# Performance work log

Hardware: AMD Instinct MI355X
Metric: run time of the kernel (lower is better)

Reference implementation:

```python
import jax, jax.numpy as jnp
import numpy as np

S, D_IN, D_OUT = 4096, 1024, 1024

def setup_inputs() -> dict:
    key = jax.random.key(0)
    kx, kq, kk, kv = jax.random.split(key, 4)
    scale = 0.02
    return {
        "x": jax.random.normal(kx, (S, D_IN), dtype=jnp.float32),
        "W_query": jax.random.normal(kq, (D_IN, D_OUT), dtype=jnp.float32) * scale,
        "W_key": jax.random.normal(kk, (D_IN, D_OUT), dtype=jnp.float32) * scale,
        "W_value": jax.random.normal(kv, (D_IN, D_OUT), dtype=jnp.float32) * scale,
    }

def reference(x, W_query, W_key, W_value):
    # x: [S, d_in]; W_*: [d_in, d_out]
    queries = x @ W_query        # [S, d_out]
    keys = x @ W_key             # [S, d_out]
    values = x @ W_value         # [S, d_out]
    d_k = keys.shape[-1]
    attn_scores = queries @ keys.T            # [S, S]
    attn_weights = jax.nn.softmax(attn_scores / jnp.sqrt(jnp.float32(d_k)), axis=-1)
    context_vec = attn_weights @ values       # [S, d_out]
    return context_vec
```

## Files before the change

kernel.cpp:

```cpp
#include <hip/hip_runtime.h>

typedef _Float16 f16x8 __attribute__((ext_vector_type(8)));
typedef float f32x4 __attribute__((ext_vector_type(4)));
typedef unsigned short u16;
typedef u16 u16x8 __attribute__((ext_vector_type(8)));
typedef u16 u16x4 __attribute__((ext_vector_type(4)));

__device__ __forceinline__ u16 f2h_bits(float f) {
    _Float16 h = (_Float16)f;
    return __builtin_bit_cast(u16, h);
}
__device__ __forceinline__ float h2f(u16 b) {
    return (float)__builtin_bit_cast(_Float16, b);
}

typedef __attribute__((address_space(1))) unsigned int gu32_as1;
typedef __attribute__((address_space(3))) unsigned int lu32_as3;
__device__ __forceinline__ void gload16(const u16* g, u16* l) {
    __builtin_amdgcn_global_load_lds((gu32_as1*)g, (lu32_as3*)l, 16, 0, 0);
}

template <int MODE>
__global__ __launch_bounds__(512, 2) void gemm_bt(
    const u16* __restrict__ A, int lda,
    const u16* __restrict__ B, int ldb,
    u16* __restrict__ C, int ldc,
    int Ksplit, float alpha, size_t c_z_stride,
    int bnW, int bmW, int numPanelX,
    float* __restrict__ rowsum, u16* __restrict__ vt)
{
    __shared__ __attribute__((aligned(16))) u16 As[32768];
    __shared__ __attribute__((aligned(16))) u16 Bs[32768];

    const int t    = threadIdx.x;
    const int lane = t & 63;
    const int wave = t >> 6;
    const int wm   = wave >> 2;
    const int wn   = wave & 3;
    const int l16  = lane & 15;
    const int quad = lane >> 4;

    const int lin = blockIdx.y * gridDim.x + blockIdx.x;
    const int xcd = lin & 7;
    const int idx = lin >> 3;
    const int px  = xcd % numPanelX;
    const int py  = xcd / numPanelX;
    const int bn  = px * bnW + idx % bnW;
    const int bm  = py * bmW + idx / bnW;

    const int kz = blockIdx.z;
    A += (size_t)kz * Ksplit;
    B += (size_t)kz * Ksplit;
    C += (size_t)kz * c_z_stride;

    const int srow = t >> 2;
    const int sseg = ((t & 3) ^ ((t >> 3) & 3)) * 8;

    const u16* Ag = A + (size_t)(bm * 256 + srow) * lda + sseg;
    const u16* Bg = B + (size_t)(bn * 256 + srow) * ldb + sseg;
    const size_t a128 = (size_t)128 * lda;
    const size_t b128 = (size_t)128 * ldb;

    u16* AsD = &As[t * 8];
    u16* BsD = &Bs[t * 8];

#define STAGE(bufv, kt) do {                                       \
        const u16* _ga = Ag + (size_t)(kt) * 32;                   \
        const u16* _gb = Bg + (size_t)(kt) * 32;                   \
        u16* _la = AsD + (bufv) * 8192;                            \
        u16* _lb = BsD + (bufv) * 8192;                            \
        gload16(_ga,        _la);              \
        gload16(_ga + a128, _la + 4096);       \
        gload16(_gb,        _lb);              \
        gload16(_gb + b128, _lb + 4096);       \
    } while (0)

    const int fslot = (quad ^ ((l16 >> 1) & 3)) * 8;
    const u16* Afr = &As[wm * 4096 + l16 * 32 + fslot];
    const u16* Bfr = &Bs[wn * 2048 + l16 * 32 + fslot];

    f32x4 acc[8][4] = {};

    const int NT = Ksplit >> 5;

    STAGE(0, 0);
    STAGE(1, 1);
    STAGE(2, 2);
    asm volatile("s_waitcnt vmcnt(8)" ::: "memory");
    __builtin_amdgcn_s_barrier();
    asm volatile("" ::: "memory");

    for (int k = 0; k < NT; ++k) {
        const int buf = k & 3;

        f16x8 af[8], bf[4];
#pragma unroll
        for (int mi = 0; mi < 8; mi++)
            af[mi] = *(const f16x8*)(Afr + buf * 8192 + mi * 512);
#pragma unroll
        for (int nj = 0; nj < 4; nj++)
            bf[nj] = *(const f16x8*)(Bfr + buf * 8192 + nj * 512);

        if (k + 3 < NT) STAGE((k + 3) & 3, k + 3);

#pragma unroll
        for (int mi = 0; mi < 8; mi++)
#pragma unroll
            for (int nj = 0; nj < 4; nj++)
                acc[mi][nj] = __builtin_amdgcn_mfma_f32_16x16x32_f16(
                    af[mi], bf[nj], acc[mi][nj], 0, 0, 0);

        if (k < NT - 3)       asm volatile("s_waitcnt vmcnt(8)" ::: "memory");
        else if (k == NT - 3) asm volatile("s_waitcnt vmcnt(4)" ::: "memory");
        else if (k == NT - 2) asm volatile("s_waitcnt vmcnt(0)" ::: "memory");
        __builtin_amdgcn_s_barrier();
        asm volatile("" ::: "memory");
    }
#undef STAGE

    const int crow = bm * 256 + wm * 128 + quad * 4;
    const int ccol = bn * 256 + wn * 64 + l16;

    if (MODE == 1) {
        float rs[8][4];
#pragma unroll
        for (int mi = 0; mi < 8; mi++)
#pragma unroll
            for (int r = 0; r < 4; r++) rs[mi][r] = 0.f;
#pragma unroll
        for (int mi = 0; mi < 8; mi++) {
#pragma unroll
            for (int ni = 0; ni < 4; ni++) {
#pragma unroll
                for (int r = 0; r < 4; r++) {
                    float e = __expf(acc[mi][ni][r] * alpha);
                    rs[mi][r] += e;
                    C[(size_t)(crow + mi * 16 + r) * ldc + (ccol + ni * 16)] = f2h_bits(e);
                }
            }
        }
#pragma unroll
        for (int mi = 0; mi < 8; mi++) {
#pragma unroll
            for (int r = 0; r < 4; r++) {
                float s = rs[mi][r];
#pragma unroll
                for (int o = 1; o < 16; o <<= 1) s += __shfl_xor(s, o);
                if (l16 == 0)
                    atomicAdd(&rowsum[crow + mi * 16 + r], s);
            }
        }
    } else if (MODE == 2 && bn >= 8) {
#pragma unroll
        for (int ni = 0; ni < 4; ni++) {
            const int cV = (bn - 8) * 256 + wn * 64 + ni * 16 + l16;
#pragma unroll
            for (int mi = 0; mi < 8; mi++) {
                u16x4 o;
#pragma unroll
                for (int r = 0; r < 4; r++) o[r] = f2h_bits(acc[mi][ni][r]);
                *(u16x4*)(vt + (size_t)cV * 4096 + crow + mi * 16) = o;
            }
        }
    } else {
#pragma unroll
        for (int mi = 0; mi < 8; mi++)
#pragma unroll
            for (int ni = 0; ni < 4; ni++)
#pragma unroll
                for (int r = 0; r < 4; r++)
                    C[(size_t)(crow + mi * 16 + r) * ldc + (ccol + ni * 16)] =
                        f2h_bits(acc[mi][ni][r] * alpha);
    }
}

__global__ __launch_bounds__(256) void cast_to_f16(
    const float* __restrict__ in, u16* __restrict__ out, int n)
{
    int i = (blockIdx.x * 256 + threadIdx.x) * 4;
    if (i + 3 < n) {
        float4 v = *(const float4*)(in + i);
        ushort4 o;
        o.x = f2h_bits(v.x);
        o.y = f2h_bits(v.y);
        o.z = f2h_bits(v.z);
        o.w = f2h_bits(v.w);
        *(ushort4*)(out + i) = o;
    }
}

__global__ __launch_bounds__(256) void transpose_w3(
    const float* __restrict__ W0, const float* __restrict__ W1,
    const float* __restrict__ W2, u16* __restrict__ out)
{
    const float* in = (blockIdx.z == 0) ? W0 : (blockIdx.z == 1) ? W1 : W2;
    u16* o = out + (size_t)blockIdx.z * 1024 * 1024;
    __shared__ float tile[32][33];
    const int bx = blockIdx.x * 32;
    const int by = blockIdx.y * 32;
    const int tx = threadIdx.x, ty = threadIdx.y;
#pragma unroll
    for (int j = 0; j < 4; j++)
        tile[ty + j * 8][tx] = in[(size_t)(by + ty + j * 8) * 1024 + bx + tx];
    __syncthreads();
#pragma unroll
    for (int j = 0; j < 4; j++)
        o[(size_t)(bx + ty + j * 8) * 1024 + by + tx] = f2h_bits(tile[tx][ty + j * 8]);
}

__global__ __launch_bounds__(256) void zero_f32(float* __restrict__ p, int n)
{
    int i = (blockIdx.x * 256 + threadIdx.x) * 4;
    if (i + 3 < n) *(float4*)(p + i) = float4{0.f, 0.f, 0.f, 0.f};
}

__global__ __launch_bounds__(256) void add_div4(
    const u16* __restrict__ P, const float* __restrict__ l,
    float* __restrict__ o)
{
    const size_t zs = (size_t)4096 * 1024;
    int i = (blockIdx.x * 256 + threadIdx.x) * 8;
    float inv = 1.0f / l[i >> 10];
    float s[8] = {};
#pragma unroll
    for (int z = 0; z < 4; z++) {
        u16x8 h = *(const u16x8*)(P + z * zs + i);
#pragma unroll
        for (int j = 0; j < 8; j++) s[j] += h2f(h[j]);
    }
    float4 lo{s[0] * inv, s[1] * inv, s[2] * inv, s[3] * inv};
    float4 hi{s[4] * inv, s[5] * inv, s[6] * inv, s[7] * inv};
    *(float4*)(o + i) = lo;
    *(float4*)(o + i + 4) = hi;
}

extern "C" void kernel_launch(void* const* d_in, const int* in_sizes, int n_in,
                              void* d_out, int out_size, void* d_ws, size_t ws_size,
                              hipStream_t stream)
{
    (void)in_sizes; (void)n_in; (void)out_size; (void)ws_size;
    const float* x  = (const float*)d_in[0];
    const float* Wq = (const float*)d_in[1];
    const float* Wk = (const float*)d_in[2];
    const float* Wv = (const float*)d_in[3];
    float* out = (float*)d_out;
    char* ws = (char*)d_ws;

    u16* xb  = (u16*)(ws);
    u16* Wt  = (u16*)(ws + ((size_t)8  << 20));
    u16* QK  = (u16*)(ws + ((size_t)14 << 20));
    u16* Sb  = (u16*)(ws + ((size_t)32 << 20));
    u16* Vt  = (u16*)(ws + ((size_t)64 << 20));
    float* lr = (float*)(ws + ((size_t)72 << 20));
    u16* P   = (u16*)(ws);

    const int S = 4096, D = 1024;
    dim3 tb(32, 8);

    cast_to_f16<<<(S * D) / (4 * 256), 256, 0, stream>>>(x, xb, S * D);

    transpose_w3<<<dim3(32, 32, 3), tb, 0, stream>>>(Wq, Wk, Wv, Wt);

    gemm_bt<2><<<dim3(12, 16, 1), 512, 0, stream>>>(
        xb, D, Wt, D, QK, 2048, D, 1.0f, 0, 3, 8, 4, nullptr, Vt);

    zero_f32<<<S / (4 * 256), 256, 0, stream>>>(lr, S);

    gemm_bt<1><<<dim3(16, 16, 1), 512, 0, stream>>>(
        QK, 2048, QK + 1024, 2048, Sb, S, D, 0.03125f, 0, 4, 8, 4, lr, nullptr);

    gemm_bt<0><<<dim3(4, 16, 4), 512, 0, stream>>>(
        Sb, S, Vt, S, P, D, 1024, 1.0f, (size_t)S * D, 1, 8, 4, nullptr, nullptr);

    add_div4<<<(S * D) / (8 * 256), 256, 0, stream>>>(P, lr, out);
}
```

Measured before the change: 216.4 us.

## Restructure GEMM main loop into 8-phase ping-pong schedule with K=64 tiles

```diff
diff --git a/kernel.cpp b/kernel.cpp
--- a/kernel.cpp
+++ b/kernel.cpp
@@ -19,6 +19,13 @@
 __device__ __forceinline__ void gload16(const u16* g, u16* l) {
     __builtin_amdgcn_global_load_lds((gu32_as1*)g, (lu32_as3*)l, 16, 0, 0);
 }
+
+#define BAR   __builtin_amdgcn_s_barrier()
+#define LGK0  asm volatile("s_waitcnt lgkmcnt(0)" ::: "memory")
+#define VM4   asm volatile("s_waitcnt vmcnt(4)" ::: "memory")
+#define VM0   asm volatile("s_waitcnt vmcnt(0)" ::: "memory")
+#define PRIO1 __builtin_amdgcn_s_setprio(1)
+#define PRIO0 __builtin_amdgcn_s_setprio(0)
 
 template <int MODE>
 __global__ __launch_bounds__(512, 2) void gemm_bt(
@@ -53,70 +60,101 @@
     B += (size_t)kz * Ksplit;
     C += (size_t)kz * c_z_stride;
 
-    const int srow = t >> 2;
-    const int sseg = ((t & 3) ^ ((t >> 3) & 3)) * 8;
-
+    const int srow = t >> 3;
+    const int sseg = ((t & 7) ^ ((t >> 3) & 7)) * 8;
     const u16* Ag = A + (size_t)(bm * 256 + srow) * lda + sseg;
     const u16* Bg = B + (size_t)(bn * 256 + srow) * ldb + sseg;
-    const size_t a128 = (size_t)128 * lda;
-    const size_t b128 = (size_t)128 * ldb;
-
     u16* AsD = &As[t * 8];
     u16* BsD = &Bs[t * 8];
 
-#define STAGE(bufv, kt) do {                                       \
-        const u16* _ga = Ag + (size_t)(kt) * 32;                   \
-        const u16* _gb = Bg + (size_t)(kt) * 32;                   \
-        u16* _la = AsD + (bufv) * 8192;                            \
-        u16* _lb = BsD + (bufv) * 8192;                            \
-        gload16(_ga,        _la);              \
-        gload16(_ga + a128, _la + 4096);       \
-        gload16(_gb,        _lb);              \
-        gload16(_gb + b128, _lb + 4096);       \
+#define STG_A(h, bufv, kt) do {                                         \
+        const u16* _s = Ag + (size_t)(h) * 128 * lda + (size_t)(kt) * 64; \
+        u16* _d = AsD + (bufv) * 16384 + (h) * 8192;                    \
+        gload16(_s, _d);                                                \
+        gload16(_s + (size_t)64 * lda, _d + 4096);                      \
     } while (0)
-
-    const int fslot = (quad ^ ((l16 >> 1) & 3)) * 8;
-    const u16* Afr = &As[wm * 4096 + l16 * 32 + fslot];
-    const u16* Bfr = &Bs[wn * 2048 + l16 * 32 + fslot];
+#define STG_B(h, bufv, kt) do {                                         \
+        const u16* _s = Bg + (size_t)(h) * 128 * ldb + (size_t)(kt) * 64; \
+        u16* _d = BsD + (bufv) * 16384 + (h) * 8192;                    \
+        gload16(_s, _d);                                                \
+        gload16(_s + (size_t)64 * ldb, _d + 4096);                      \
+    } while (0)
+
+    const int skz = l16 & 7;
+    const int sk0 = (quad ^ skz) * 8;
+    const int sk1 = ((4 + quad) ^ skz) * 8;
+    const u16* Ab = As + wm * 8192 + l16 * 64;
+    const u16* Bb = Bs + (wn >> 1) * 8192 + (wn & 1) * 4096 + l16 * 64;
+
+#define RD_A(dst, mh, bufv) do {                                        \
+        _Pragma("unroll") for (int mi = 0; mi < 4; mi++) {              \
+            dst[mi][0] = *(const f16x8*)(Ab + (bufv) * 16384 +          \
+                                         (mh) * 4096 + mi * 1024 + sk0);\
+            dst[mi][1] = *(const f16x8*)(Ab + (bufv) * 16384 +          \
+                                         (mh) * 4096 + mi * 1024 + sk1);\
+        } } while (0)
+#define RD_B(dst, nh, bufv) do {                                        \
+        _Pragma("unroll") for (int nj = 0; nj < 2; nj++) {              \
+            dst[nj][0] = *(const f16x8*)(Bb + (bufv) * 16384 +          \
+                                         (nh) * 2048 + nj * 1024 + sk0);\
+            dst[nj][1] = *(const f16x8*)(Bb + (bufv) * 16384 +          \
+                                         (nh) * 2048 + nj * 1024 + sk1);\
+        } } while (0)
+#define MFQ(mh, nh, Af, Bf) do {                                        \
+        _Pragma("unroll") for (int mi = 0; mi < 4; mi++)                \
+        _Pragma("unroll") for (int nj = 0; nj < 2; nj++)                \
+        _Pragma("unroll") for (int kk = 0; kk < 2; kk++)                \
+            acc[(mh)*4+mi][(nh)*2+nj] =                                 \
+                __builtin_amdgcn_mfma_f32_16x16x32_f16(                 \
+                    Af[mi][kk], Bf[nj][kk], acc[(mh)*4+mi][(nh)*2+nj],  \
+                    0, 0, 0);                                           \
+    } while (0)
 
     f32x4 acc[8][4] = {};
-
-    const int NT = Ksplit >> 5;
-
-    STAGE(0, 0);
-    STAGE(1, 1);
-    STAGE(2, 2);
-    asm volatile("s_waitcnt vmcnt(8)" ::: "memory");
-    __builtin_amdgcn_s_barrier();
-    asm volatile("" ::: "memory");
-
-    for (int k = 0; k < NT; ++k) {
-        const int buf = k & 3;
-
-        f16x8 af[8], bf[4];
-#pragma unroll
-        for (int mi = 0; mi < 8; mi++)
-            af[mi] = *(const f16x8*)(Afr + buf * 8192 + mi * 512);
-#pragma unroll
-        for (int nj = 0; nj < 4; nj++)
-            bf[nj] = *(const f16x8*)(Bfr + buf * 8192 + nj * 512);
-
-        if (k + 3 < NT) STAGE((k + 3) & 3, k + 3);
-
-#pragma unroll
-        for (int mi = 0; mi < 8; mi++)
-#pragma unroll
-            for (int nj = 0; nj < 4; nj++)
-                acc[mi][nj] = __builtin_amdgcn_mfma_f32_16x16x32_f16(
-                    af[mi], bf[nj], acc[mi][nj], 0, 0, 0);
-
-        if (k < NT - 3)       asm volatile("s_waitcnt vmcnt(8)" ::: "memory");
-        else if (k == NT - 3) asm volatile("s_waitcnt vmcnt(4)" ::: "memory");
-        else if (k == NT - 2) asm volatile("s_waitcnt vmcnt(0)" ::: "memory");
-        __builtin_amdgcn_s_barrier();
-        asm volatile("" ::: "memory");
+    const int NI = Ksplit >> 7;
+
+    STG_A(0, 0, 0); STG_A(1, 0, 0); STG_B(0, 0, 0); STG_B(1, 0, 0);
+    STG_B(0, 1, 1); STG_B(1, 1, 1);
+    VM4;
+    BAR;
+
+    for (int it = 0; it < NI; ++it) {
+        const int t0 = it * 2, t1 = it * 2 + 1;
+        const bool nl = (it + 1 < NI);
+        f16x8 a0[4][2], a1[4][2], b0[2][2], b1[2][2];
+
+        RD_A(a0, 0, 0); RD_B(b0, 0, 0);
+        STG_A(0, 1, t1);
+        BAR; LGK0; PRIO1; MFQ(0, 0, a0, b0); PRIO0; BAR;
+        RD_B(b1, 1, 0);
+        STG_A(1, 1, t1);
+        BAR; LGK0; PRIO1; MFQ(0, 1, a0, b1); PRIO0; BAR;
+        RD_A(a1, 1, 0);
+        if (nl) STG_B(0, 0, t0 + 2);
+        BAR; LGK0; PRIO1; MFQ(1, 0, a1, b0); PRIO0; BAR;
+        if (nl) STG_B(1, 0, t0 + 2);
+        BAR; LGK0; PRIO1; MFQ(1, 1, a1, b1); PRIO0;
+        if (nl) VM4; else VM0;
+        BAR;
+        RD_A(a0, 0, 1); RD_B(b0, 0, 1);
+        if (nl) STG_A(0, 0, t0 + 2);
+        BAR; LGK0; PRIO1; MFQ(0, 0, a0, b0); PRIO0; BAR;
+        RD_B(b1, 1, 1);
+        if (nl) STG_A(1, 0, t0 + 2);
+        BAR; LGK0; PRIO1; MFQ(0, 1, a0, b1); PRIO0; BAR;
+        RD_A(a1, 1, 1);
+        if (nl) STG_B(0, 1, t1 + 2);
+        BAR; LGK0; PRIO1; MFQ(1, 0, a1, b0); PRIO0; BAR;
+        if (nl) STG_B(1, 1, t1 + 2);
+        BAR; LGK0; PRIO1; MFQ(1, 1, a1, b1); PRIO0;
+        if (nl) VM4; else VM0;
+        BAR;
     }
-#undef STAGE
+#undef STG_A
+#undef STG_B
+#undef RD_A
+#undef RD_B
+#undef MFQ
 
     const int crow = bm * 256 + wm * 128 + quad * 4;
     const int ccol = bn * 256 + wn * 64 + l16;
```

Result: no change. 216.4 us (-0.0%).
